# Kernel tuning notes

Measured on AMD Instinct MI355X. Metric: run time of the kernel, lower is better.

Reference implementation:

```python
import jax, jax.numpy as jnp
import numpy as np

MIN_WEIGHT = 0.0
MAX_WEIGHT = 500.0


def setup_inputs() -> dict:
    key = jax.random.key(0)
    k1, k2, k3 = jax.random.split(key, 3)
    B, P = 131072, 64   # groundings, predicates
    C, L = 128, 3       # clauses, literals per clause
    ground_atoms = jax.random.normal(k1, (B, P), dtype=jnp.float32)
    # learned clause weights, initial_clause_weight = 0.5
    clause_weights = 0.5 * jnp.ones((C,), dtype=jnp.float32)
    # which predicate each literal refers to
    literal_idx = jax.random.randint(k2, (C, L), 0, P, dtype=jnp.int64)
    # 0 -> negated literal (sign -1), 1 -> positive literal (sign +1)
    sign_bits = jax.random.randint(k3, (C, L), 0, 2, dtype=jnp.int32)
    return {
        "ground_atoms": ground_atoms,
        "clause_weights": clause_weights,
        "literal_idx": literal_idx,
        "sign_bits": sign_bits,
    }


def reference(ground_atoms, clause_weights, literal_idx, sign_bits):
    """Vectorized KnowledgeEnhancer forward.

    Per clause (GodelBoostConormApprox):
      literals = signs * ground_atoms[:, idx]
      delta    = signs * clamp(w) * softmax(literals)
    Then concat all clause deltas and scatter_add into predicate space.
    """
    B, P = ground_atoms.shape
    C, L = literal_idx.shape
    signs = (2 * sign_bits - 1).astype(ground_atoms.dtype)  # [C, L] in {-1,+1}
    gathered = ground_atoms[:, literal_idx]                 # [B, C, L] gather
    literals = signs[None, :, :] * gathered                 # signed pre-activations
    w = jnp.clip(clause_weights, MIN_WEIGHT, MAX_WEIGHT)    # [C]
    delta = signs[None, :, :] * w[None, :, None] * jax.nn.softmax(literals, axis=-1)
    # concat over clauses (dim=1 in the torch code) then scatter_add over predicates
    delta_flat = delta.reshape(B, C * L)
    idx_flat = literal_idx.reshape(C * L)
    out = jax.ops.segment_sum(delta_flat.T, idx_flat, num_segments=P)  # [P, B]
    return out.T  # [B, P]
```

## Files before the change

### kernel.cpp

```cpp
#include <hip/hip_runtime.h>
#include <stdint.h>

typedef unsigned int  u32;
typedef unsigned short u16;

#define B_ROWS 131072
#define P_PRED 64
#define C_CLS  128
#define NPAIR  384
#define CAP    32
#define RPB    128
#define TPB    512
#define GCAP   104
#define LOG2E  1.4426950408889634f

#if __has_builtin(__builtin_amdgcn_exp2f)
#define EXP2F(x) __builtin_amdgcn_exp2f(x)
#else
#define EXP2F(x) exp2f(x)
#endif

#if __has_builtin(__builtin_amdgcn_rcpf)
#define RCPF(x) __builtin_amdgcn_rcpf(x)
#else
#define RCPF(x) (1.0f / (x))
#endif

__device__ __forceinline__ float bf16_to_f(u16 u) {
    return __uint_as_float(((u32)u) << 16);
}
__device__ __forceinline__ u16 f_to_bf16(float f) {
    u32 u = __float_as_uint(f);
    u += 0x7FFFu + ((u >> 16) & 1u);
    return (u16)(u >> 16);
}
__device__ __forceinline__ u32 pack_bf16x2(float lo, float hi) {
    return (u32)f_to_bf16(lo) | ((u32)f_to_bf16(hi) << 16);
}

__global__ __launch_bounds__(TPB, 8)
void ke_fused(const u32* __restrict__ lidx_w,
              const u32* __restrict__ sb_w,
              const u32* __restrict__ w_w,
              const void* __restrict__ atoms_v,
              void* __restrict__ out_v) {
    __shared__ u32 S[8192];
    __shared__ uint2 srec[8 * GCAP];
    __shared__ unsigned char cnt8[P_PRED];
    u16* E2 = (u16*)S;

    const int tid = threadIdx.x;
    const int lane = tid & 63;
    const int g = __builtin_amdgcn_readfirstlane(tid >> 6);
    const int rowBase = blockIdx.x * RPB;

    int*   scnt  = (int*)&S[0];
    int*   det   = (int*)&S[64];
    int*   sidx  = (int*)&S[128];
    int*   ssb   = (int*)&S[512];
    u32*   recPk = &S[1024];
    float* recW  = (float*)&S[3072];

    if (tid < P_PRED) scnt[tid] = 0;
    if (tid < 3) det[tid] = 1;
    __syncthreads();
    if (tid < NPAIR / 2) {
        if (lidx_w[2 * tid + 1] != 0u) det[0] = 0;
        if (sb_w[2 * tid + 1]   != 0u) det[1] = 0;
    }
    if (tid == 0 && (w_w[0] & 0xFFFFu) == 0u) det[2] = 0;
    __syncthreads();
    if (tid < NPAIR) {
        sidx[tid] = (int)(det[0] ? lidx_w[2 * tid] : lidx_w[tid]);
        ssb[tid]  = (int)(det[1] ? sb_w[2 * tid]   : sb_w[tid]);
    }
    __syncthreads();
    const bool bf16m = (det[2] != 0);
    if (tid < NPAIR) {
        const int c = tid / 3;
        const int l = tid - c * 3;
        const int base = c * 3;
        const int o1 = base + (l == 0 ? 1 : 0);
        const int o2 = base + (l == 2 ? 1 : 2);
        const int p = sidx[tid];
        const int slot = atomicAdd(&scnt[p], 1);
        float wraw = bf16m ? bf16_to_f((u16)(w_w[c / 2] >> ((c & 1) * 16)))
                           : __uint_as_float(w_w[c]);
        float wc = fminf(fmaxf(wraw, 0.0f), 500.0f);
        if (slot < CAP) {
            u32 s1 = 2u * (u32)sidx[o1] + (ssb[o1] ? 0u : 1u);
            u32 s2 = 2u * (u32)sidx[o2] + (ssb[o2] ? 0u : 1u);
            recPk[p * CAP + slot] = (ssb[tid] ? 0u : 1u) | (s1 << 8) | (s2 << 16);
            recW[p * CAP + slot]  = ssb[tid] ? wc : -wc;
        }
    }
    __syncthreads();
    if (tid < P_PRED) {
        const int p = tid;
        const int gg = p >> 3;
        const int n = min(scnt[p], CAP);
        int off = 0;
        for (int pb = gg * 8; pb < p; ++pb) off += min(scnt[pb], CAP);
        int ncl = 0;
        for (int j = 0; j < n; ++j) {
            if (off + j < GCAP) {
                srec[gg * GCAP + off + j] =
                    make_uint2(recPk[p * CAP + j], __float_as_uint(recW[p * CAP + j]));
                ++ncl;
            }
        }
        cnt8[p] = (unsigned char)ncl;
    }
    __syncthreads();

    {
        const int a = tid & 63;
        const int c0 = (tid >> 6) * 8;
        if (bf16m) {
            const u16* gp0 = (const u16*)atoms_v + (size_t)(rowBase + 2 * a) * P_PRED + c0;
            uint4 v0 = *(const uint4*)gp0;
            uint4 v1 = *(const uint4*)(gp0 + P_PRED);
            u32 w0[4] = {v0.x, v0.y, v0.z, v0.w};
            u32 w1[4] = {v1.x, v1.y, v1.z, v1.w};
#pragma unroll
            for (int k = 0; k < 4; ++k) {
                float xl0 = __uint_as_float(w0[k] << 16) * LOG2E;
                float xh0 = __uint_as_float(w0[k] & 0xFFFF0000u) * LOG2E;
                float xl1 = __uint_as_float(w1[k] << 16) * LOG2E;
                float xh1 = __uint_as_float(w1[k] & 0xFFFF0000u) * LOG2E;
                float el0 = EXP2F(xl0), eh0 = EXP2F(xh0);
                float el1 = EXP2F(xl1), eh1 = EXP2F(xh1);
                const int m = c0 + 2 * k;
                S[(2 * m)     * 64 + a] = pack_bf16x2(el0, el1);
                S[(2 * m + 1) * 64 + a] = pack_bf16x2(RCPF(el0), RCPF(el1));
                S[(2 * m + 2) * 64 + a] = pack_bf16x2(eh0, eh1);
                S[(2 * m + 3) * 64 + a] = pack_bf16x2(RCPF(eh0), RCPF(eh1));
            }
        } else {
            const float* gp0 = (const float*)atoms_v + (size_t)(rowBase + 2 * a) * P_PRED + c0;
            float4 u0 = *(const float4*)gp0;
            float4 u1 = *(const float4*)(gp0 + 4);
            float4 d0 = *(const float4*)(gp0 + P_PRED);
            float4 d1 = *(const float4*)(gp0 + P_PRED + 4);
            float r0[8] = {u0.x, u0.y, u0.z, u0.w, u1.x, u1.y, u1.z, u1.w};
            float r1[8] = {d0.x, d0.y, d0.z, d0.w, d1.x, d1.y, d1.z, d1.w};
#pragma unroll
            for (int k = 0; k < 8; ++k) {
                float e0 = EXP2F(r0[k] * LOG2E);
                float e1 = EXP2F(r1[k] * LOG2E);
                const int m = c0 + k;
                S[(2 * m)     * 64 + a] = pack_bf16x2(e0, e1);
                S[(2 * m + 1) * 64 + a] = pack_bf16x2(RCPF(e0), RCPF(e1));
            }
        }
    }
    __syncthreads();

    const int q2 = 2 * lane;
    float2 acc[8];
    int j = g * GCAP;

#pragma unroll
    for (int pp = 0; pp < 8; ++pp) {
        const int p = g * 8 + pp;
        const u32 eppv = *(const u32*)&E2[(2 * p)     * RPB + q2];
        const u32 epnv = *(const u32*)&E2[(2 * p + 1) * RPB + q2];
        const float eppx = __uint_as_float(eppv << 16);
        const float eppy = __uint_as_float(eppv & 0xFFFF0000u);
        const float epnx = __uint_as_float(epnv << 16);
        const float epny = __uint_as_float(epnv & 0xFFFF0000u);
        const int n = (int)cnt8[p];
        float2 a0 = make_float2(0.0f, 0.0f);
        float2 a1 = make_float2(0.0f, 0.0f);

#define REC_BODY(J, A)                                                        \
        {                                                                     \
            const uint2 rec = srec[J];                     \
            const u32 pk = rec.x;                                             \
            const float sw = __uint_as_float(rec.y);                          \
            const u32 s1v = *(const u32*)&E2[(int)((pk >> 8)  & 255u) * RPB + q2]; \
            const u32 s2v = *(const u32*)&E2[(int)((pk >> 16) & 255u) * RPB + q2]; \
            const float ssx = (pk & 1u) ? epnx : eppx;                        \
            const float ssy = (pk & 1u) ? epny : eppy;                        \
            const float s1x = __uint_as_float(s1v << 16);                     \
            const float s1y = __uint_as_float(s1v & 0xFFFF0000u);             \
            const float s2x = __uint_as_float(s2v << 16);                     \
            const float s2y = __uint_as_float(s2v & 0xFFFF0000u);             \
            const float tx = RCPF(ssx + s1x + s2x);                           \
            const float ty = RCPF(ssy + s1y + s2y);                          \
            A.x = fmaf(sw * ssx, tx, A.x);                                    \
            A.y = fmaf(sw * ssy, ty, A.y);                                    \
        }

        int e = 0;
        for (; e + 3 < n; e += 4) {
            REC_BODY(j,     a0)
            REC_BODY(j + 1, a1)
            REC_BODY(j + 2, a0)
            REC_BODY(j + 3, a1)
            j += 4;
        }
        for (; e < n; ++e, ++j) REC_BODY(j, a0)
#undef REC_BODY
        acc[pp] = make_float2(a0.x + a1.x, a0.y + a1.y);
    }

    if (bf16m) {
        u16* op0 = (u16*)out_v + (size_t)(rowBase + q2) * P_PRED + g * 8;
        u16* op1 = op0 + P_PRED;
        uint4 o0, o1v;
        o0.x  = pack_bf16x2(acc[0].x, acc[1].x);
        o0.y  = pack_bf16x2(acc[2].x, acc[3].x);
        o0.z  = pack_bf16x2(acc[4].x, acc[5].x);
        o0.w  = pack_bf16x2(acc[6].x, acc[7].x);
        o1v.x = pack_bf16x2(acc[0].y, acc[1].y);
        o1v.y = pack_bf16x2(acc[2].y, acc[3].y);
        o1v.z = pack_bf16x2(acc[4].y, acc[5].y);
        o1v.w = pack_bf16x2(acc[6].y, acc[7].y);
        *(uint4*)op0 = o0;
        *(uint4*)op1 = o1v;
    } else {
        float* op0 = (float*)out_v + (size_t)(rowBase + q2) * P_PRED + g * 8;
        float* op1 = op0 + P_PRED;
        *(float4*)(op0)     = make_float4(acc[0].x, acc[1].x, acc[2].x, acc[3].x);
        *(float4*)(op0 + 4) = make_float4(acc[4].x, acc[5].x, acc[6].x, acc[7].x);
        *(float4*)(op1)     = make_float4(acc[0].y, acc[1].y, acc[2].y, acc[3].y);
        *(float4*)(op1 + 4) = make_float4(acc[4].y, acc[5].y, acc[6].y, acc[7].y);
    }
}

extern "C" void kernel_launch(void* const* d_in, const int* in_sizes, int n_in,
                              void* d_out, int out_size, void* d_ws, size_t ws_size,
                              hipStream_t stream_h) {
    const u32* clause_weights = (const u32*)d_in[1];
    const u32* literal_idx    = (const u32*)d_in[2];
    const u32* sign_bits      = (const u32*)d_in[3];
    (void)d_ws; (void)ws_size;

    ke_fused<<<B_ROWS / RPB, TPB, 0, stream_h>>>(literal_idx, sign_bits,
                                                 clause_weights, d_in[0],
                                                 d_out);
}
```

Before: 102.6 us.

## Process four rows per lane and compute reciprocals on the fly

Doubles rows per block to 256, so each lane now handles four rows packed as bf16x4 in a uint2 LDS table. Only exp(x) is stored; the negative-literal values are recomputed with rcp when a sign bit is set, which halves the LDS table. Record fields are made wave-uniform via readfirstlane. This amortises the per-block clause-table setup over more rows and cuts LDS loads per row, in exchange for more rcp work per record, more registers, and half as many blocks (launch bounds lowered to 4).

```diff
diff --git a/kernel.cpp b/kernel.cpp
--- a/kernel.cpp
+++ b/kernel.cpp
@@ -9,7 +9,7 @@
 #define C_CLS  128
 #define NPAIR  384
 #define CAP    32
-#define RPB    128
+#define RPB    256
 #define TPB    512
 #define GCAP   104
 #define LOG2E  1.4426950408889634f
@@ -38,22 +38,22 @@
     return (u32)f_to_bf16(lo) | ((u32)f_to_bf16(hi) << 16);
 }
 
-__global__ __launch_bounds__(TPB, 8)
+__global__ __launch_bounds__(TPB, 4)
 void ke_fused(const u32* __restrict__ lidx_w,
               const u32* __restrict__ sb_w,
               const u32* __restrict__ w_w,
               const void* __restrict__ atoms_v,
               void* __restrict__ out_v) {
-    __shared__ u32 S[8192];
+    __shared__ uint2 E1q[P_PRED * 64];
     __shared__ uint2 srec[8 * GCAP];
     __shared__ unsigned char cnt8[P_PRED];
-    u16* E2 = (u16*)S;
 
     const int tid = threadIdx.x;
     const int lane = tid & 63;
     const int g = __builtin_amdgcn_readfirstlane(tid >> 6);
     const int rowBase = blockIdx.x * RPB;
 
+    u32*   S     = (u32*)E1q;
     int*   scnt  = (int*)&S[0];
     int*   det   = (int*)&S[64];
     int*   sidx  = (int*)&S[128];
@@ -117,115 +117,123 @@
         const int a = tid & 63;
         const int c0 = (tid >> 6) * 8;
         if (bf16m) {
-            const u16* gp0 = (const u16*)atoms_v + (size_t)(rowBase + 2 * a) * P_PRED + c0;
-            uint4 v0 = *(const uint4*)gp0;
-            uint4 v1 = *(const uint4*)(gp0 + P_PRED);
+            const u16* gp = (const u16*)atoms_v + (size_t)(rowBase + 4 * a) * P_PRED + c0;
+            uint4 v0 = *(const uint4*)gp;
+            uint4 v1 = *(const uint4*)(gp + P_PRED);
+            uint4 v2 = *(const uint4*)(gp + 2 * P_PRED);
+            uint4 v3 = *(const uint4*)(gp + 3 * P_PRED);
             u32 w0[4] = {v0.x, v0.y, v0.z, v0.w};
             u32 w1[4] = {v1.x, v1.y, v1.z, v1.w};
+            u32 w2[4] = {v2.x, v2.y, v2.z, v2.w};
+            u32 w3[4] = {v3.x, v3.y, v3.z, v3.w};
 #pragma unroll
             for (int k = 0; k < 4; ++k) {
-                float xl0 = __uint_as_float(w0[k] << 16) * LOG2E;
-                float xh0 = __uint_as_float(w0[k] & 0xFFFF0000u) * LOG2E;
-                float xl1 = __uint_as_float(w1[k] << 16) * LOG2E;
-                float xh1 = __uint_as_float(w1[k] & 0xFFFF0000u) * LOG2E;
-                float el0 = EXP2F(xl0), eh0 = EXP2F(xh0);
-                float el1 = EXP2F(xl1), eh1 = EXP2F(xh1);
-                const int m = c0 + 2 * k;
-                S[(2 * m)     * 64 + a] = pack_bf16x2(el0, el1);
-                S[(2 * m + 1) * 64 + a] = pack_bf16x2(RCPF(el0), RCPF(el1));
-                S[(2 * m + 2) * 64 + a] = pack_bf16x2(eh0, eh1);
-                S[(2 * m + 3) * 64 + a] = pack_bf16x2(RCPF(eh0), RCPF(eh1));
+                float l0 = EXP2F(__uint_as_float(w0[k] << 16) * LOG2E);
+                float l1 = EXP2F(__uint_as_float(w1[k] << 16) * LOG2E);
+                float l2 = EXP2F(__uint_as_float(w2[k] << 16) * LOG2E);
+                float l3 = EXP2F(__uint_as_float(w3[k] << 16) * LOG2E);
+                float h0 = EXP2F(__uint_as_float(w0[k] & 0xFFFF0000u) * LOG2E);
+                float h1 = EXP2F(__uint_as_float(w1[k] & 0xFFFF0000u) * LOG2E);
+                float h2 = EXP2F(__uint_as_float(w2[k] & 0xFFFF0000u) * LOG2E);
+                float h3 = EXP2F(__uint_as_float(w3[k] & 0xFFFF0000u) * LOG2E);
+                E1q[(c0 + 2 * k)     * 64 + a] =
+                    make_uint2(pack_bf16x2(l0, l1), pack_bf16x2(l2, l3));
+                E1q[(c0 + 2 * k + 1) * 64 + a] =
+                    make_uint2(pack_bf16x2(h0, h1), pack_bf16x2(h2, h3));
             }
         } else {
-            const float* gp0 = (const float*)atoms_v + (size_t)(rowBase + 2 * a) * P_PRED + c0;
-            float4 u0 = *(const float4*)gp0;
-            float4 u1 = *(const float4*)(gp0 + 4);
-            float4 d0 = *(const float4*)(gp0 + P_PRED);
-            float4 d1 = *(const float4*)(gp0 + P_PRED + 4);
-            float r0[8] = {u0.x, u0.y, u0.z, u0.w, u1.x, u1.y, u1.z, u1.w};
-            float r1[8] = {d0.x, d0.y, d0.z, d0.w, d1.x, d1.y, d1.z, d1.w};
-#pragma unroll
-            for (int k = 0; k < 8; ++k) {
-                float e0 = EXP2F(r0[k] * LOG2E);
-                float e1 = EXP2F(r1[k] * LOG2E);
-                const int m = c0 + k;
-                S[(2 * m)     * 64 + a] = pack_bf16x2(e0, e1);
-                S[(2 * m + 1) * 64 + a] = pack_bf16x2(RCPF(e0), RCPF(e1));
-            }
-        }
-    }
-    __syncthreads();
-
-    const int q2 = 2 * lane;
-    float2 acc[8];
+            const float* gp = (const float*)atoms_v + (size_t)(rowBase + 4 * a) * P_PRED + c0;
+            float x0[8], x1[8], x2[8], x3[8];
+            *(float4*)&x0[0] = *(const float4*)gp;
+            *(float4*)&x0[4] = *(const float4*)(gp + 4);
+            *(float4*)&x1[0] = *(const float4*)(gp + P_PRED);
+            *(float4*)&x1[4] = *(const float4*)(gp + P_PRED + 4);
+            *(float4*)&x2[0] = *(const float4*)(gp + 2 * P_PRED);
+            *(float4*)&x2[4] = *(const float4*)(gp + 2 * P_PRED + 4);
+            *(float4*)&x3[0] = *(const float4*)(gp + 3 * P_PRED);
+            *(float4*)&x3[4] = *(const float4*)(gp + 3 * P_PRED + 4);
+#pragma unroll
+            for (int m = 0; m < 8; ++m) {
+                float e0 = EXP2F(x0[m] * LOG2E);
+                float e1 = EXP2F(x1[m] * LOG2E);
+                float e2 = EXP2F(x2[m] * LOG2E);
+                float e3 = EXP2F(x3[m] * LOG2E);
+                E1q[(c0 + m) * 64 + a] =
+                    make_uint2(pack_bf16x2(e0, e1), pack_bf16x2(e2, e3));
+            }
+        }
+    }
+    __syncthreads();
+
+    float ac[8][4];
     int j = g * GCAP;
 
 #pragma unroll
     for (int pp = 0; pp < 8; ++pp) {
         const int p = g * 8 + pp;
-        const u32 eppv = *(const u32*)&E2[(2 * p)     * RPB + q2];
-        const u32 epnv = *(const u32*)&E2[(2 * p + 1) * RPB + q2];
-        const float eppx = __uint_as_float(eppv << 16);
-        const float eppy = __uint_as_float(eppv & 0xFFFF0000u);
-        const float epnx = __uint_as_float(epnv << 16);
-        const float epny = __uint_as_float(epnv & 0xFFFF0000u);
+        const uint2 eq = E1q[p * 64 + lane];
+        float ep[4] = {__uint_as_float(eq.x << 16),
+                       __uint_as_float(eq.x & 0xFFFF0000u),
+                       __uint_as_float(eq.y << 16),
+                       __uint_as_float(eq.y & 0xFFFF0000u)};
+        float en[4] = {RCPF(ep[0]), RCPF(ep[1]), RCPF(ep[2]), RCPF(ep[3])};
         const int n = (int)cnt8[p];
-        float2 a0 = make_float2(0.0f, 0.0f);
-        float2 a1 = make_float2(0.0f, 0.0f);
-
-#define REC_BODY(J, A)                                                        \
-        {                                                                     \
-            const uint2 rec = srec[J];                     \
-            const u32 pk = rec.x;                                             \
-            const float sw = __uint_as_float(rec.y);                          \
-            const u32 s1v = *(const u32*)&E2[(int)((pk >> 8)  & 255u) * RPB + q2]; \
-            const u32 s2v = *(const u32*)&E2[(int)((pk >> 16) & 255u) * RPB + q2]; \
-            const float ssx = (pk & 1u) ? epnx : eppx;                        \
-            const float ssy = (pk & 1u) ? epny : eppy;                        \
-            const float s1x = __uint_as_float(s1v << 16);                     \
-            const float s1y = __uint_as_float(s1v & 0xFFFF0000u);             \
-            const float s2x = __uint_as_float(s2v << 16);                     \
-            const float s2y = __uint_as_float(s2v & 0xFFFF0000u);             \
-            const float tx = RCPF(ssx + s1x + s2x);                           \
-            const float ty = RCPF(ssy + s1y + s2y);                          \
-            A.x = fmaf(sw * ssx, tx, A.x);                                    \
-            A.y = fmaf(sw * ssy, ty, A.y);                                    \
-        }
-
-        int e = 0;
-        for (; e + 3 < n; e += 4) {
-            REC_BODY(j,     a0)
-            REC_BODY(j + 1, a1)
-            REC_BODY(j + 2, a0)
-            REC_BODY(j + 3, a1)
-            j += 4;
-        }
-        for (; e < n; ++e, ++j) REC_BODY(j, a0)
-#undef REC_BODY
-        acc[pp] = make_float2(a0.x + a1.x, a0.y + a1.y);
-    }
-
+        float a0[4] = {0.0f, 0.0f, 0.0f, 0.0f};
+
+        for (int e = 0; e < n; ++e, ++j) {
+            const uint2 rec = srec[j];
+            const u32 pk = (u32)__builtin_amdgcn_readfirstlane((int)rec.x);
+            const float sw = __uint_as_float(
+                (u32)__builtin_amdgcn_readfirstlane((int)rec.y));
+            const u32 sl1 = (pk >> 8) & 255u;
+            const u32 sl2 = (pk >> 16) & 255u;
+            const uint2 q1 = E1q[(int)(sl1 >> 1) * 64 + lane];
+            const uint2 q2 = E1q[(int)(sl2 >> 1) * 64 + lane];
+            float s1[4] = {__uint_as_float(q1.x << 16),
+                           __uint_as_float(q1.x & 0xFFFF0000u),
+                           __uint_as_float(q1.y << 16),
+                           __uint_as_float(q1.y & 0xFFFF0000u)};
+            float s2[4] = {__uint_as_float(q2.x << 16),
+                           __uint_as_float(q2.x & 0xFFFF0000u),
+                           __uint_as_float(q2.y << 16),
+                           __uint_as_float(q2.y & 0xFFFF0000u)};
+            if (sl1 & 1u) {
+#pragma unroll
+                for (int r = 0; r < 4; ++r) s1[r] = RCPF(s1[r]);
+            }
+            if (sl2 & 1u) {
+#pragma unroll
+                for (int r = 0; r < 4; ++r) s2[r] = RCPF(s2[r]);
+            }
+#pragma unroll
+            for (int r = 0; r < 4; ++r) {
+                const float ssr = (pk & 1u) ? en[r] : ep[r];
+                const float t = RCPF(ssr + s1[r] + s2[r]);
+                a0[r] = fmaf(sw * ssr, t, a0[r]);
+            }
+        }
+#pragma unroll
+        for (int r = 0; r < 4; ++r) ac[pp][r] = a0[r];
+    }
+
+    const int row0 = rowBase + 4 * lane;
     if (bf16m) {
-        u16* op0 = (u16*)out_v + (size_t)(rowBase + q2) * P_PRED + g * 8;
-        u16* op1 = op0 + P_PRED;
-        uint4 o0, o1v;
-        o0.x  = pack_bf16x2(acc[0].x, acc[1].x);
-        o0.y  = pack_bf16x2(acc[2].x, acc[3].x);
-        o0.z  = pack_bf16x2(acc[4].x, acc[5].x);
-        o0.w  = pack_bf16x2(acc[6].x, acc[7].x);
-        o1v.x = pack_bf16x2(acc[0].y, acc[1].y);
-        o1v.y = pack_bf16x2(acc[2].y, acc[3].y);
-        o1v.z = pack_bf16x2(acc[4].y, acc[5].y);
-        o1v.w = pack_bf16x2(acc[6].y, acc[7].y);
-        *(uint4*)op0 = o0;
-        *(uint4*)op1 = o1v;
+#pragma unroll
+        for (int r = 0; r < 4; ++r) {
+            uint4 o;
+            o.x = pack_bf16x2(ac[0][r], ac[1][r]);
+            o.y = pack_bf16x2(ac[2][r], ac[3][r]);
+            o.z = pack_bf16x2(ac[4][r], ac[5][r]);
+            o.w = pack_bf16x2(ac[6][r], ac[7][r]);
+            *(uint4*)((u16*)out_v + (size_t)(row0 + r) * P_PRED + g * 8) = o;
+        }
     } else {
-        float* op0 = (float*)out_v + (size_t)(rowBase + q2) * P_PRED + g * 8;
-        float* op1 = op0 + P_PRED;
-        *(float4*)(op0)     = make_float4(acc[0].x, acc[1].x, acc[2].x, acc[3].x);
-        *(float4*)(op0 + 4) = make_float4(acc[4].x, acc[5].x, acc[6].x, acc[7].x);
-        *(float4*)(op1)     = make_float4(acc[0].y, acc[1].y, acc[2].y, acc[3].y);
-        *(float4*)(op1 + 4) = make_float4(acc[4].y, acc[5].y, acc[6].y, acc[7].y);
+#pragma unroll
+        for (int r = 0; r < 4; ++r) {
+            float* op = (float*)out_v + (size_t)(row0 + r) * P_PRED + g * 8;
+            *(float4*)(op)     = make_float4(ac[0][r], ac[1][r], ac[2][r], ac[3][r]);
+            *(float4*)(op + 4) = make_float4(ac[4][r], ac[5][r], ac[6][r], ac[7][r]);
+        }
     }
 }
 
```

Result: slower. 109.9 us (+7.0%).
